# Performance work log

Measured on AMD Instinct MI355X. Metric: run time of the kernel, lower is better.

Reference implementation:

```python
import jax, jax.numpy as jnp
import numpy as np

IN_DIMS = (8, 8, 8, 8)
OUT_DIMS = (8, 8, 8, 8)
RANK = 8
IN_FEATURES = 4096
OUT_FEATURES = 4096
BATCH = 4096


def setup_inputs() -> dict:
    key = jax.random.key(0)
    ks = jax.random.split(key, 6)
    scale = 1.0 / (IN_FEATURES ** 0.5)
    d = len(IN_DIMS)
    ranks = (1,) + (RANK,) * (d - 1) + (1,)
    cores = {}
    for k in range(d):
        shape = (ranks[k], IN_DIMS[k], OUT_DIMS[k], ranks[k + 1])
        # roughly balanced per-core scale so the dense-equivalent weight has ~1/sqrt(N) scale
        c_scale = scale ** (1.0 / d)
        cores[f"core_{k}"] = (jax.random.normal(ks[k + 1], shape, dtype=jnp.float32) * c_scale)
    x = jax.random.normal(ks[0], (BATCH, IN_FEATURES), dtype=jnp.float32)
    bias = jnp.zeros((OUT_FEATURES,), dtype=jnp.float32)
    return {"x": x, **cores, "bias": bias}


def _tt_contract(x, cores):
    # x: (B, N) with N = prod(IN_DIMS). Cores: core_k (r_{k-1}, i_k, o_k, r_k).
    # y[b, o1..od] = sum_{i,r} prod_k core_k[r_{k-1}, i_k, o_k, r_k] * x[b, i1..id]
    B = x.shape[0]
    d = len(IN_DIMS)
    # z: (Bo, r, i_k, suffix) where Bo = B * prod(out dims already contracted)
    z = x.reshape(B, 1, IN_DIMS[0], -1)
    for k, core in enumerate(cores):
        # contract current input mode and left rank against the core
        z = jnp.einsum("bris,riok->boks", z, core)  # (Bo, o_k, r_k, suffix)
        if k + 1 < d:
            Bo, ok, rk, s = z.shape
            z = z.reshape(Bo * ok, rk, IN_DIMS[k + 1], s // IN_DIMS[k + 1])
    return z.reshape(B, -1)  # (B, prod(OUT_DIMS))


def reference(x, core_0, core_1, core_2, core_3, bias):
    in_dtype = x.dtype
    xc = x.astype(core_0.dtype)
    y = _tt_contract(xc, (core_0, core_1, core_2, core_3))
    y = y + bias
    return y.astype(in_dtype)
```

## Files before the change

### kernel.cpp

```cpp
#include <hip/hip_runtime.h>
#include <hip/hip_bf16.h>


typedef __attribute__((ext_vector_type(8))) short bf16x8;
typedef __attribute__((ext_vector_type(16))) float f32x16;

#define MFMA32(a, b, c) __builtin_amdgcn_mfma_f32_32x32x16_bf16(a, b, c, 0, 0, 0)

__device__ __forceinline__ unsigned short bfu(float f) {
    __hip_bfloat16 h = __float2bfloat16(f);
    return *reinterpret_cast<unsigned short*>(&h);
}
__device__ __forceinline__ unsigned pk2(float a, float b) {
    return (unsigned)bfu(a) | ((unsigned)bfu(b) << 16);
}

__device__ __forceinline__ void gload_lds16(const char* g, char* l) {
    __builtin_amdgcn_global_load_lds(
        (const __attribute__((address_space(1))) unsigned int*)g,
        (__attribute__((address_space(3))) unsigned int*)l,
        16, 0, 0);
}

__global__ void tt_prep(const float* __restrict__ c0, const float* __restrict__ c1,
                        const float* __restrict__ c2, const float* __restrict__ c3,
                        unsigned short* __restrict__ wpack) {
    int e    = blockIdx.x * 256 + threadIdx.x;
    int lane = (e >> 3) & 63;
    int j    = e & 7;
    int hi   = lane >> 5, l31 = lane & 31;
    float acc = 0.f;
    if (e < 32768) {
        int idx = e;
        int r2  = idx >> 12;
        int nt  = (idx >> 11) & 1;
        int ks1 = (idx >> 9) & 3;
        int i23 = ks1 * 16 + hi * 8 + j;
        int o23 = nt * 32 + l31;
        int i2 = i23 >> 3, i3 = i23 & 7, o2 = o23 >> 3, o3 = o23 & 7;
        #pragma unroll
        for (int r3 = 0; r3 < 8; ++r3)
            acc += c2[((r2 * 8 + i2) * 8 + o2) * 8 + r3] * c3[(r3 * 8 + i3) * 8 + o3];
    } else {
        int idx = e - 32768;
        int r2  = idx >> 12;
        int mt2 = (idx >> 11) & 1;
        int kt  = (idx >> 10) & 1;
        int ks2 = (idx >> 9) & 1;
        int i01 = kt * 32 + ks2 * 16 + hi * 8 + j;
        int o01 = mt2 * 32 + l31;
        int i0 = i01 >> 3, i1 = i01 & 7, o0 = o01 >> 3, o1 = o01 & 7;
        #pragma unroll
        for (int r1 = 0; r1 < 8; ++r1)
            acc += c0[(i0 * 8 + o0) * 8 + r1] * c1[((r1 * 8 + i1) * 8 + o1) * 8 + r2];
    }
    wpack[e] = bfu(acc);
}

__device__ __forceinline__ void stage_r2(const char* wp, char* sm, int r2,
                                         int wave, int lane) {
    int isU = wave >> 1;
    int f0  = (wave & 1) * 4;
    const char* src = wp + isU * 65536 + (r2 * 8 + f0) * 1024 + lane * 16;
    char* dst = sm + isU * 8192 + f0 * 1024;
    #pragma unroll
    for (int i = 0; i < 4; ++i)
        gload_lds16(src + i * 1024, dst + i * 1024);
}

__global__ __launch_bounds__(256, 3)
void tt_main(const float* __restrict__ x, const float* __restrict__ bias,
             const unsigned short* __restrict__ wpack, float* __restrict__ out) {
    __shared__ __attribute__((aligned(16))) char smem[2][16384];
    const int lane = threadIdx.x & 63;
    const int wave = threadIdx.x >> 6;
    const int b    = blockIdx.x * 4 + wave;
    const int l31  = lane & 31;
    const int hi   = lane >> 5;
    const char* wp = (const char*)wpack;

    stage_r2(wp, smem[0], 0, wave, lane);

    const float* xb = x + (size_t)b * 4096;
    bf16x8 xa[2][4];
    #pragma unroll
    for (int mt = 0; mt < 2; ++mt)
        #pragma unroll
        for (int ks1 = 0; ks1 < 4; ++ks1) {
            const float* p = xb + (mt * 32 + l31) * 64 + ks1 * 16 + hi * 8;
            float4 u0 = *(const float4*)p;
            float4 u1 = *(const float4*)(p + 4);
            union { unsigned w[4]; bf16x8 v; } t;
            t.w[0] = pk2(u0.x, u0.y);
            t.w[1] = pk2(u0.z, u0.w);
            t.w[2] = pk2(u1.x, u1.y);
            t.w[3] = pk2(u1.z, u1.w);
            xa[mt][ks1] = t.v;
        }

    f32x16 yacc[2][2];
    #pragma unroll
    for (int i = 0; i < 2; ++i)
        #pragma unroll
        for (int k = 0; k < 2; ++k)
            yacc[i][k] = (f32x16)0.0f;

    __syncthreads();

    #pragma unroll
    for (int r2 = 0; r2 < 8; ++r2) {
        const char* cur = smem[r2 & 1];
        char*       nxt = smem[(r2 & 1) ^ 1];
        if (r2 < 7)
            stage_r2(wp, nxt, r2 + 1, wave, lane);

        const char* vb = cur + lane * 16;
        const char* ub = cur + 8192 + lane * 16;

        #pragma unroll
        for (int mt = 0; mt < 2; ++mt) {
            bf16x8 uf[2][2];
            #pragma unroll
            for (int mt2 = 0; mt2 < 2; ++mt2)
                #pragma unroll
                for (int ks2 = 0; ks2 < 2; ++ks2)
                    uf[mt2][ks2] = *(const bf16x8*)(ub + (((mt2 * 2 + mt) * 2 + ks2) << 10));

            #pragma unroll
            for (int nt = 0; nt < 2; ++nt) {
                f32x16 s = (f32x16)0.0f;
                #pragma unroll
                for (int ks1 = 0; ks1 < 4; ++ks1)
                    s = MFMA32(xa[mt][ks1],
                               *(const bf16x8*)(vb + ((nt * 4 + ks1) << 10)), s);

                bf16x8 bf[2];
                #pragma unroll
                for (int ks2 = 0; ks2 < 2; ++ks2) {
                    unsigned A0 = pk2(s[8 * ks2 + 0], s[8 * ks2 + 1]);
                    unsigned B0 = pk2(s[8 * ks2 + 2], s[8 * ks2 + 3]);
                    unsigned A1 = pk2(s[8 * ks2 + 4], s[8 * ks2 + 5]);
                    unsigned B1 = pk2(s[8 * ks2 + 6], s[8 * ks2 + 7]);
                    auto rA = __builtin_amdgcn_permlane32_swap((int)A0, (int)A1, false, false);
                    auto rB = __builtin_amdgcn_permlane32_swap((int)B0, (int)B1, false, false);
                    union { unsigned w[4]; bf16x8 v; } t;
                    t.w[0] = (unsigned)rA[0];
                    t.w[1] = (unsigned)rB[0];
                    t.w[2] = (unsigned)rA[1];
                    t.w[3] = (unsigned)rB[1];
                    bf[ks2] = t.v;
                }

                #pragma unroll
                for (int mt2 = 0; mt2 < 2; ++mt2)
                    #pragma unroll
                    for (int ks2 = 0; ks2 < 2; ++ks2)
                        yacc[mt2][nt] = MFMA32(uf[mt2][ks2], bf[ks2], yacc[mt2][nt]);
            }
        }
        __syncthreads();
    }

    float* ob = out + (size_t)b * 4096;
    #pragma unroll
    for (int mt2 = 0; mt2 < 2; ++mt2)
        #pragma unroll
        for (int nt = 0; nt < 2; ++nt)
            #pragma unroll
            for (int r = 0; r < 16; ++r) {
                int o01 = mt2 * 32 + (r & 3) + 8 * (r >> 2) + 4 * hi;
                int o23 = nt * 32 + l31;
                int off = o01 * 64 + o23;
                ob[off] = yacc[mt2][nt][r] + bias[off];
            }
}

extern "C" void kernel_launch(void* const* d_in, const int* in_sizes, int n_in,
                              void* d_out, int out_size, void* d_ws, size_t ws_size,
                              hipStream_t stream) {
    const float* x    = (const float*)d_in[0];
    const float* c0   = (const float*)d_in[1];
    const float* c1   = (const float*)d_in[2];
    const float* c2   = (const float*)d_in[3];
    const float* c3   = (const float*)d_in[4];
    const float* bias = (const float*)d_in[5];
    unsigned short* wpack = (unsigned short*)d_ws;

    tt_prep<<<256, 256, 0, stream>>>(c0, c1, c2, c3, wpack);
    tt_main<<<1024, 256, 0, stream>>>(x, bias, wpack, (float*)d_out);
}
```

Before: 162.9 us.

## Stage weights in two halves with 8-wave blocks, dropping per-r2 barriers

```diff
diff --git a/kernel.cpp b/kernel.cpp
--- a/kernel.cpp
+++ b/kernel.cpp
@@ -57,29 +57,30 @@
     wpack[e] = bfu(acc);
 }
 
-__device__ __forceinline__ void stage_r2(const char* wp, char* sm, int r2,
-                                         int wave, int lane) {
-    int isU = wave >> 1;
-    int f0  = (wave & 1) * 4;
-    const char* src = wp + isU * 65536 + (r2 * 8 + f0) * 1024 + lane * 16;
-    char* dst = sm + isU * 8192 + f0 * 1024;
+__device__ __forceinline__ void stage_half(const char* wp, char* sm, int h,
+                                           int wave, int lane) {
     #pragma unroll
-    for (int i = 0; i < 4; ++i)
-        gload_lds16(src + i * 1024, dst + i * 1024);
+    for (int i = 0; i < 8; ++i) {
+        int isU = i >> 2;
+        const char* src = wp + isU * 65536 + h * 32768 + (i & 3) * 8192
+                          + wave * 1024 + lane * 16;
+        char* dst = sm + i * 8192 + wave * 1024;
+        gload_lds16(src, dst);
+    }
 }
 
-__global__ __launch_bounds__(256, 3)
+__global__ __launch_bounds__(512, 2)
 void tt_main(const float* __restrict__ x, const float* __restrict__ bias,
              const unsigned short* __restrict__ wpack, float* __restrict__ out) {
-    __shared__ __attribute__((aligned(16))) char smem[2][16384];
+    __shared__ __attribute__((aligned(16))) char smem[65536];
     const int lane = threadIdx.x & 63;
     const int wave = threadIdx.x >> 6;
-    const int b    = blockIdx.x * 4 + wave;
+    const int b    = blockIdx.x * 8 + wave;
     const int l31  = lane & 31;
     const int hi   = lane >> 5;
     const char* wp = (const char*)wpack;
 
-    stage_r2(wp, smem[0], 0, wave, lane);
+    stage_half(wp, smem, 0, wave, lane);
 
     const float* xb = x + (size_t)b * 4096;
     bf16x8 xa[2][4];
@@ -107,58 +108,63 @@
 
     __syncthreads();
 
+    const char* VL = smem;
+    const char* UL = smem + 32768;
+
     #pragma unroll
-    for (int r2 = 0; r2 < 8; ++r2) {
-        const char* cur = smem[r2 & 1];
-        char*       nxt = smem[(r2 & 1) ^ 1];
-        if (r2 < 7)
-            stage_r2(wp, nxt, r2 + 1, wave, lane);
-
-        const char* vb = cur + lane * 16;
-        const char* ub = cur + 8192 + lane * 16;
-
+    for (int h = 0; h < 2; ++h) {
+        if (h == 1) {
+            __syncthreads();
+            stage_half(wp, smem, 1, wave, lane);
+            __syncthreads();
+        }
         #pragma unroll
-        for (int mt = 0; mt < 2; ++mt) {
-            bf16x8 uf[2][2];
+        for (int r2h = 0; r2h < 4; ++r2h) {
             #pragma unroll
-            for (int mt2 = 0; mt2 < 2; ++mt2)
-                #pragma unroll
-                for (int ks2 = 0; ks2 < 2; ++ks2)
-                    uf[mt2][ks2] = *(const bf16x8*)(ub + (((mt2 * 2 + mt) * 2 + ks2) << 10));
-
-            #pragma unroll
-            for (int nt = 0; nt < 2; ++nt) {
-                f32x16 s = (f32x16)0.0f;
-                #pragma unroll
-                for (int ks1 = 0; ks1 < 4; ++ks1)
-                    s = MFMA32(xa[mt][ks1],
-                               *(const bf16x8*)(vb + ((nt * 4 + ks1) << 10)), s);
-
-                bf16x8 bf[2];
-                #pragma unroll
-                for (int ks2 = 0; ks2 < 2; ++ks2) {
-                    unsigned A0 = pk2(s[8 * ks2 + 0], s[8 * ks2 + 1]);
-                    unsigned B0 = pk2(s[8 * ks2 + 2], s[8 * ks2 + 3]);
-                    unsigned A1 = pk2(s[8 * ks2 + 4], s[8 * ks2 + 5]);
-                    unsigned B1 = pk2(s[8 * ks2 + 6], s[8 * ks2 + 7]);
-                    auto rA = __builtin_amdgcn_permlane32_swap((int)A0, (int)A1, false, false);
-                    auto rB = __builtin_amdgcn_permlane32_swap((int)B0, (int)B1, false, false);
-                    union { unsigned w[4]; bf16x8 v; } t;
-                    t.w[0] = (unsigned)rA[0];
-                    t.w[1] = (unsigned)rB[0];
-                    t.w[2] = (unsigned)rA[1];
-                    t.w[3] = (unsigned)rB[1];
-                    bf[ks2] = t.v;
-                }
-
+            for (int mt = 0; mt < 2; ++mt) {
+                bf16x8 uf[2][2];
                 #pragma unroll
                 for (int mt2 = 0; mt2 < 2; ++mt2)
                     #pragma unroll
                     for (int ks2 = 0; ks2 < 2; ++ks2)
-                        yacc[mt2][nt] = MFMA32(uf[mt2][ks2], bf[ks2], yacc[mt2][nt]);
+                        uf[mt2][ks2] = *(const bf16x8*)(UL +
+                            ((((r2h * 2 + mt2) * 2 + mt) * 2 + ks2) << 10) + lane * 16);
+
+                #pragma unroll
+                for (int nt = 0; nt < 2; ++nt) {
+                    f32x16 s = (f32x16)0.0f;
+                    #pragma unroll
+                    for (int ks1 = 0; ks1 < 4; ++ks1)
+                        s = MFMA32(xa[mt][ks1],
+                                   *(const bf16x8*)(VL +
+                                       (((r2h * 2 + nt) * 4 + ks1) << 10) + lane * 16),
+                                   s);
+
+                    bf16x8 bf[2];
+                    #pragma unroll
+                    for (int ks2 = 0; ks2 < 2; ++ks2) {
+                        unsigned A0 = pk2(s[8 * ks2 + 0], s[8 * ks2 + 1]);
+                        unsigned B0 = pk2(s[8 * ks2 + 2], s[8 * ks2 + 3]);
+                        unsigned A1 = pk2(s[8 * ks2 + 4], s[8 * ks2 + 5]);
+                        unsigned B1 = pk2(s[8 * ks2 + 6], s[8 * ks2 + 7]);
+                        auto rA = __builtin_amdgcn_permlane32_swap((int)A0, (int)A1, false, false);
+                        auto rB = __builtin_amdgcn_permlane32_swap((int)B0, (int)B1, false, false);
+                        union { unsigned w[4]; bf16x8 v; } t;
+                        t.w[0] = (unsigned)rA[0];
+                        t.w[1] = (unsigned)rB[0];
+                        t.w[2] = (unsigned)rA[1];
+                        t.w[3] = (unsigned)rB[1];
+                        bf[ks2] = t.v;
+                    }
+
+                    #pragma unroll
+                    for (int mt2 = 0; mt2 < 2; ++mt2)
+                        #pragma unroll
+                        for (int ks2 = 0; ks2 < 2; ++ks2)
+                            yacc[mt2][nt] = MFMA32(uf[mt2][ks2], bf[ks2], yacc[mt2][nt]);
+                }
             }
         }
-        __syncthreads();
     }
 
     float* ob = out + (size_t)b * 4096;
@@ -187,5 +193,5 @@
     unsigned short* wpack = (unsigned short*)d_ws;
 
     tt_prep<<<256, 256, 0, stream>>>(c0, c1, c2, c3, wpack);
-    tt_main<<<1024, 256, 0, stream>>>(x, bias, wpack, (float*)d_out);
+    tt_main<<<512, 512, 0, stream>>>(x, bias, wpack, (float*)d_out);
 }
```

Result: faster. 145.1 us (-11.0%).
